# Kernel optimization log

Hardware: AMD Instinct MI355X
Metric: run time of the kernel (lower is better)

## Reference

```python
import jax
import jax.numpy as jnp
import numpy as np


def setup_inputs() -> dict:
    key = jax.random.key(0)
    k1, k2 = jax.random.split(key)
    B, C, H, W = 2, 256, 64, 128  # 1/8-res RAFT features of a 512x1024 image
    fmap1 = jax.random.normal(k1, (B, C, H, W), dtype=jnp.float32)
    fmap2 = jax.random.normal(k2, (B, C, H, W), dtype=jnp.float32)
    return {"fmap1": fmap1, "fmap2": fmap2, "k": 32}


def reference(fmap1, fmap2, k):
    B, C, H, W = fmap1.shape
    N = H * W
    f1 = fmap1.reshape(B, C, N)
    f2 = fmap2.reshape(B, C, N)

    # --- KNN (FAISS inner-product search), indices are non-differentiable ---
    scores = jnp.einsum('bcn,bcm->bnm', jax.lax.stop_gradient(f1),
                        jax.lax.stop_gradient(f2))  # [B, N1, N2]
    _, idx = jax.lax.top_k(scores, k)               # [B, N1, k]
    idx = jnp.transpose(idx, (0, 2, 1))             # [B, k, N1]

    # --- gather top-k target features: gathered[b,c,j,n] = f2[b,c,idx[b,j,n]] ---
    gathered = jax.vmap(lambda f, i: f[:, i])(f2, idx)  # [B, C, k, N1]

    # --- sparse correlation ---
    corr_sp = jnp.einsum('bcn,bckn->bkn', f1, gathered) / jnp.sqrt(jnp.float32(C))

    # --- coordinate grids (y-first), relative displacement ---
    ys, xs = jnp.meshgrid(jnp.arange(H, dtype=jnp.float32),
                          jnp.arange(W, dtype=jnp.float32), indexing='ij')
    coords = jnp.stack([ys.ravel(), xs.ravel()])          # [2, N], y first
    coords0 = jnp.broadcast_to(coords[None, :, None, :], (B, 2, k, N))
    coords1 = jnp.transpose(coords[:, idx], (1, 0, 2, 3))  # [B, 2, k, N]
    coords1 = coords1 - coords0                            # relative offsets

    batch_index = jnp.broadcast_to(
        jnp.arange(B, dtype=jnp.float32).reshape(B, 1, 1, 1), (B, 1, k, N))

    return corr_sp, coords0, coords1, batch_index
```

## Files before the change

kernel.cpp:

```cpp
#include <hip/hip_runtime.h>
#include <hip/hip_bf16.h>

#define B_  2
#define C_  256
#define H_  64
#define W_  128
#define N_  (H_ * W_)
#define K_  32
#define Q_  16
#define CK2 48
#define TN  32
#define TM  32
#define NHT 64

typedef short  short8  __attribute__((ext_vector_type(8)));
typedef short  short4v __attribute__((ext_vector_type(4)));
typedef float  floatx4 __attribute__((ext_vector_type(4)));

__device__ __forceinline__ unsigned umin_(unsigned a, unsigned b) { return a < b ? a : b; }
__device__ __forceinline__ unsigned umax_(unsigned a, unsigned b) { return a > b ? a : b; }
__device__ __forceinline__ ushort f2bf(float v) {
    __hip_bfloat16 h = __float2bfloat16(v);
    ushort u; __builtin_memcpy(&u, &h, 2); return u;
}
__device__ __forceinline__ unsigned med3u(unsigned a, unsigned b, unsigned c) {
    unsigned d;
    asm("v_med3_u32 %0, %1, %2, %3" : "=v"(d) : "v"(a), "v"(b), "v"(c));
    return d;
}

__device__ __forceinline__ unsigned packkey(float v, int m) {
    const float vc = v > 0.0f ? v : 0.0f;
    unsigned b; __builtin_memcpy(&b, &vc, 4);
    return (b & 0xFFFFE000u) | (unsigned)m;
}

__device__ __forceinline__ void qinsert(unsigned (&q)[Q_], unsigned k) {
#pragma unroll
    for (int i = Q_ - 1; i > 0; --i)
        q[i] = med3u(q[i - 1], k, q[i]);
    q[0] = umax_(q[0], k);
}

#define CSWAP(a, b) { const unsigned _mx = umax_(a, b); \
                      const unsigned _mn = umin_(a, b); (a) = _mx; (b) = _mn; }

__global__ void raft_prep_kernel(const float* __restrict__ f1,
                                 const float* __restrict__ f2,
                                 float* __restrict__ f1Tf,
                                 ushort* __restrict__ f2T,
                                 float* __restrict__ f2Tf) {
    __shared__ float tile[32][33];
    const int nt = blockIdx.x;
    const int ct = blockIdx.y;
    const int z  = blockIdx.z;
    const int b  = z >> 1;
    const float* __restrict__ src = (z & 1) ? f2 : f1;
    const int tid = threadIdx.x;

    {
        const int cl = tid >> 3;
        const int nx = tid & 7;
        const float4 v = *(const float4*)(
            src + ((size_t)b * C_ + (ct * 32 + cl)) * N_ + (nt * 32 + nx * 4));
        tile[cl][nx * 4 + 0] = v.x;
        tile[cl][nx * 4 + 1] = v.y;
        tile[cl][nx * 4 + 2] = v.z;
        tile[cl][nx * 4 + 3] = v.w;
    }
    __syncthreads();
    {
        const int nl = tid >> 3;
        const int c4 = (tid & 7) * 4;
        float4 v;
        v.x = tile[c4 + 0][nl];
        v.y = tile[c4 + 1][nl];
        v.z = tile[c4 + 2][nl];
        v.w = tile[c4 + 3][nl];
        const size_t o = ((size_t)b * N_ + (nt * 32 + nl)) * C_ + (ct * 32 + c4);
        if (z & 1) {
            *(float4*)(f2Tf + o) = v;
            short4v h;
            h[0] = (short)f2bf(v.x); h[1] = (short)f2bf(v.y);
            h[2] = (short)f2bf(v.z); h[3] = (short)f2bf(v.w);
            *(short4v*)(f2T + o) = h;
        } else {
            *(float4*)(f1Tf + o) = v;
        }
    }
}

__launch_bounds__(512, 4)
__global__ void raft_stage1_kernel(const float* __restrict__ f1Tf,
                                   const ushort* __restrict__ f2T,
                                   ushort* __restrict__ cand) {
    __shared__ __align__(16) ushort Bt[4][TM * 256];

    const int bid0 = blockIdx.x;
    const int bid  = ((bid0 & 7) << 6) | (bid0 >> 3);
    const int b    = bid >> 8;
    const int nt0  = (bid & 255) * TN;
    const int tid  = threadIdx.x;
    const int w    = tid >> 6;
    const int s    = w & 1;
    const int h    = w >> 1;
    const int lane = tid & 63;
    const int p    = lane & 15;
    const int q4   = lane >> 4;
    const int nrow = nt0 + s * 16 + p;
    const int mbase = h * (N_ / 4);
    const int lt   = tid & 127;

    short8 af[8];
    {
        const float* __restrict__ arow = f1Tf + ((size_t)b * N_ + nrow) * C_;
        #pragma unroll
        for (int ks = 0; ks < 8; ++ks) {
            const float4 x = *(const float4*)(arow + ks * 32 + q4 * 8);
            const float4 y = *(const float4*)(arow + ks * 32 + q4 * 8 + 4);
            short8 t;
            t[0] = (short)f2bf(x.x); t[1] = (short)f2bf(x.y);
            t[2] = (short)f2bf(x.z); t[3] = (short)f2bf(x.w);
            t[4] = (short)f2bf(y.x); t[5] = (short)f2bf(y.y);
            t[6] = (short)f2bf(y.z); t[7] = (short)f2bf(y.w);
            af[ks] = t;
        }
    }

    unsigned q[Q_];
    #pragma unroll
    for (int i = 0; i < Q_; ++i) q[i] = 0u;

    const ushort* __restrict__ Bb = f2T + (size_t)b * N_ * C_ + (size_t)mbase * C_;

    short8 stg[8];
    #pragma unroll
    for (int i = 0; i < 8; ++i) {
        const int idx = lt + 128 * i;
        const int r   = idx >> 5;
        const int c8  = idx & 31;
        stg[i] = *(const short8*)(Bb + (size_t)r * C_ + c8 * 8);
    }

    for (int mt = 0; mt < NHT; ++mt) {
        {
            ushort* __restrict__ dst = Bt[h];
            #pragma unroll
            for (int i = 0; i < 8; ++i) {
                const int idx = lt + 128 * i;
                const int r   = idx >> 5;
                const int c8  = idx & 31;
                *(short8*)(&dst[(r * 32 + (c8 ^ (r & 7))) * 8]) = stg[i];
            }
        }
        __syncthreads();

        if (mt < NHT - 1) {
            const ushort* __restrict__ src = Bb + (size_t)(mt + 1) * TM * C_;
            #pragma unroll
            for (int i = 0; i < 8; ++i) {
                const int idx = lt + 128 * i;
                const int r   = idx >> 5;
                const int c8  = idx & 31;
                stg[i] = *(const short8*)(src + (size_t)r * C_ + c8 * 8);
            }
        }

        const ushort* __restrict__ cur = Bt[h];
        floatx4 acc[2];
        #pragma unroll
        for (int f = 0; f < 2; ++f) acc[f] = (floatx4){0.f, 0.f, 0.f, 0.f};
        #pragma unroll
        for (int ks = 0; ks < 8; ++ks) {
            #pragma unroll
            for (int f = 0; f < 2; ++f) {
                const short8 bm = *(const short8*)(
                    &cur[((f * 16 + p) * 32 + ((ks * 4 + q4) ^ (p & 7))) * 8]);
                acc[f] = __builtin_amdgcn_mfma_f32_16x16x32_bf16(bm, af[ks], acc[f], 0, 0, 0);
            }
        }

        const int m0 = mbase + mt * TM;
        #pragma unroll
        for (int f = 0; f < 2; ++f) {
            const int mb = m0 + f * 16 + q4 * 4;
            unsigned k0 = packkey(acc[f][0], mb + 0);
            unsigned k1 = packkey(acc[f][1], mb + 1);
            unsigned k2 = packkey(acc[f][2], mb + 2);
            unsigned k3 = packkey(acc[f][3], mb + 3);
            CSWAP(k0, k1); CSWAP(k2, k3); CSWAP(k0, k2); CSWAP(k1, k3); CSWAP(k1, k2);
            qinsert(q, k0);
            if (__any(k1 > q[Q_ - 1])) {
                qinsert(q, k1);
                if (__any(k2 > q[Q_ - 1])) {
                    qinsert(q, k2);
                    if (__any(k3 > q[Q_ - 1])) qinsert(q, k3);
                }
            }
        }
        __syncthreads();
    }

    unsigned* __restrict__ mg = (unsigned*)&Bt[0][0];
    const int rowl = s * 16 + p;
    const int qi   = h * 4 + q4;
    #pragma unroll
    for (int t = 0; t < Q_; ++t)
        mg[(qi * Q_ + t) * 33 + rowl] = q[t];
    __syncthreads();

    unsigned* __restrict__ ms = mg + 8448;
    if (tid < 128) {
        const int r = tid >> 2, g = tid & 3;
        const unsigned* __restrict__ Lb = &mg[(g * 4) * Q_ * 33];
        unsigned* __restrict__ O = &ms[(g * 48) * 33 + r];
        int i0 = 0, i1 = 0, i2 = 0, i3 = 0;
        for (int t = 0; t < 48; ++t) {
            const unsigned a0 = (i0 < Q_) ? Lb[(0 * Q_ + i0) * 33 + r] : 0u;
            const unsigned a1 = (i1 < Q_) ? Lb[(1 * Q_ + i1) * 33 + r] : 0u;
            const unsigned a2 = (i2 < Q_) ? Lb[(2 * Q_ + i2) * 33 + r] : 0u;
            const unsigned a3 = (i3 < Q_) ? Lb[(3 * Q_ + i3) * 33 + r] : 0u;
            const unsigned m01 = umax_(a0, a1), m23 = umax_(a2, a3);
            const unsigned mx  = umax_(m01, m23);
            O[t * 33] = mx;
            i0 += (a0 == mx);
            i1 += (a0 != mx) & (a1 == mx);
            i2 += (a0 != mx) & (a1 != mx) & (a2 == mx);
            i3 += (a0 != mx) & (a1 != mx) & (a2 != mx) & (a3 == mx);
        }
    }
    __syncthreads();

    if (tid < 32) {
        int i0 = 0, i1 = 0, i2 = 0, i3 = 0;
        ushort* __restrict__ myc = cand + ((size_t)(b * N_ + nt0 + tid)) * CK2;
        for (int t = 0; t < 48; ++t) {
            const unsigned a0 = ms[(0 * 48 + i0) * 33 + tid];
            const unsigned a1 = ms[(1 * 48 + i1) * 33 + tid];
            const unsigned a2 = ms[(2 * 48 + i2) * 33 + tid];
            const unsigned a3 = ms[(3 * 48 + i3) * 33 + tid];
            const unsigned m01 = umax_(a0, a1), m23 = umax_(a2, a3);
            const unsigned mx  = umax_(m01, m23);
            myc[t] = (ushort)(mx & 0x1FFFu);
            i0 += (a0 == mx);
            i1 += (a0 != mx) & (a1 == mx);
            i2 += (a0 != mx) & (a1 != mx) & (a2 == mx);
            i3 += (a0 != mx) & (a1 != mx) & (a2 != mx) & (a3 == mx);
        }
    }
}

__launch_bounds__(64)
__global__ void raft_rerank_kernel(const float* __restrict__ f1Tf,
                                   const float* __restrict__ f2Tf,
                                   const ushort* __restrict__ cand,
                                   float* __restrict__ out) {
    __shared__ float  aS[C_];
    __shared__ float  cs[CK2];
    __shared__ ushort cmS[CK2];
    const int row = blockIdx.x;
    const int b   = row >> 13;
    const int n   = row & (N_ - 1);
    const int tid = threadIdx.x;

    if (tid < CK2) cmS[tid] = cand[(size_t)row * CK2 + tid];
    *(float4*)(&aS[tid * 4]) = *(const float4*)(f1Tf + ((size_t)b * N_ + n) * C_ + tid * 4);
    __syncthreads();

    if (tid < CK2) {
        const int m = cmS[tid];
        const float* __restrict__ bRow = f2Tf + ((size_t)b * N_ + m) * C_;
        float acc = 0.0f;
        for (int c4 = 0; c4 < C_; c4 += 4) {
            const float4 b4 = *(const float4*)(bRow + c4);
            acc = fmaf(aS[c4 + 0], b4.x, acc);
            acc = fmaf(aS[c4 + 1], b4.y, acc);
            acc = fmaf(aS[c4 + 2], b4.z, acc);
            acc = fmaf(aS[c4 + 3], b4.w, acc);
        }
        cs[tid] = acc;
    }
    __syncthreads();

    const int y0 = n >> 7, x0 = n & 127;
    if (tid < CK2) {
        const float v = cs[tid];
        const int m = cmS[tid];
        int rank = 0;
        for (int j = 0; j < CK2; ++j) {
            const float vj = cs[j];
            rank += (vj > v) || ((vj == v) && (cmS[j] < m));
        }
        if (rank < K_) {
            const size_t posn = (size_t)rank * N_ + n;
            out[(size_t)b * (K_ * N_) + posn] = v * 0.0625f;
            const size_t c1b = (size_t)1572864 + (size_t)b * 2 * K_ * N_;
            out[c1b + posn]                     = (float)((m >> 7) - y0);
            out[c1b + (size_t)(K_ * N_) + posn] = (float)((m & 127) - x0);
        }
    }
    if (tid < K_) {
        const size_t posn = (size_t)tid * N_ + n;
        const size_t c0b = (size_t)524288 + (size_t)b * 2 * K_ * N_;
        out[c0b + posn]                     = (float)y0;
        out[c0b + (size_t)(K_ * N_) + posn] = (float)x0;
        out[(size_t)2621440 + (size_t)b * (K_ * N_) + posn] = (float)b;
    }
}

extern "C" void kernel_launch(void* const* d_in, const int* in_sizes, int n_in,
                              void* d_out, int out_size, void* d_ws, size_t ws_size,
                              hipStream_t stream) {
    const float* f1 = (const float*)d_in[0];
    const float* f2 = (const float*)d_in[1];

    float*  f1Tf = (float*)d_ws;
    float*  f2Tf = f1Tf + (size_t)B_ * N_ * C_;
    ushort* f2T  = (ushort*)(f2Tf + (size_t)B_ * N_ * C_);
    ushort* cand = f2T + (size_t)B_ * N_ * C_;

    raft_prep_kernel<<<dim3(N_ / 32, C_ / 32, B_ * 2), dim3(256), 0, stream>>>(
        f1, f2, f1Tf, f2T, f2Tf);

    raft_stage1_kernel<<<dim3(B_ * (N_ / TN)), dim3(512), 0, stream>>>(f1Tf, f2T, cand);

    raft_rerank_kernel<<<dim3(B_ * N_), dim3(64), 0, stream>>>(f1Tf, f2Tf, cand,
                                                               (float*)d_out);
}
```

Before: 378.8 us.

## Shrink rerank candidates, batch rows per rerank block, relax stage1 barriers

The candidate count passed from the bf16 MFMA stage to the fp32 rerank drops from 48 to 36, which shrinks the merge loops and the rerank work. The rerank kernel now handles 16 rows per 576-thread block instead of one row per 64-thread block, with a swizzled block index. In stage 1 the first barrier moves after the next-tile global prefetch, and both barriers become a raw LDS-wait plus s_barrier. Fewer candidates raise the chance that a true top-32 neighbour is lost to bf16 rounding in the first pass.

```diff
diff --git a/kernel.cpp b/kernel.cpp
--- a/kernel.cpp
+++ b/kernel.cpp
@@ -8,10 +8,11 @@
 #define N_  (H_ * W_)
 #define K_  32
 #define Q_  16
-#define CK2 48
+#define CK2 36
 #define TN  32
 #define TM  32
 #define NHT 64
+#define RR  16
 
 typedef short  short8  __attribute__((ext_vector_type(8)));
 typedef short  short4v __attribute__((ext_vector_type(4)));
@@ -44,6 +45,13 @@
 
 #define CSWAP(a, b) { const unsigned _mx = umax_(a, b); \
                       const unsigned _mn = umin_(a, b); (a) = _mx; (b) = _mn; }
+
+__device__ __forceinline__ void bar_lgkm() {
+    asm volatile("s_waitcnt lgkmcnt(0)" ::: "memory");
+    __builtin_amdgcn_sched_barrier(0);
+    __builtin_amdgcn_s_barrier();
+    __builtin_amdgcn_sched_barrier(0);
+}
 
 __global__ void raft_prep_kernel(const float* __restrict__ f1,
                                  const float* __restrict__ f2,
@@ -153,7 +161,6 @@
                 *(short8*)(&dst[(r * 32 + (c8 ^ (r & 7))) * 8]) = stg[i];
             }
         }
-        __syncthreads();
 
         if (mt < NHT - 1) {
             const ushort* __restrict__ src = Bb + (size_t)(mt + 1) * TM * C_;
@@ -165,6 +172,7 @@
                 stg[i] = *(const short8*)(src + (size_t)r * C_ + c8 * 8);
             }
         }
+        bar_lgkm();
 
         const ushort* __restrict__ cur = Bt[h];
         floatx4 acc[2];
@@ -198,7 +206,7 @@
                 }
             }
         }
-        __syncthreads();
+        bar_lgkm();
     }
 
     unsigned* __restrict__ mg = (unsigned*)&Bt[0][0];
@@ -213,9 +221,9 @@
     if (tid < 128) {
         const int r = tid >> 2, g = tid & 3;
         const unsigned* __restrict__ Lb = &mg[(g * 4) * Q_ * 33];
-        unsigned* __restrict__ O = &ms[(g * 48) * 33 + r];
+        unsigned* __restrict__ O = &ms[(g * CK2) * 33 + r];
         int i0 = 0, i1 = 0, i2 = 0, i3 = 0;
-        for (int t = 0; t < 48; ++t) {
+        for (int t = 0; t < CK2; ++t) {
             const unsigned a0 = (i0 < Q_) ? Lb[(0 * Q_ + i0) * 33 + r] : 0u;
             const unsigned a1 = (i1 < Q_) ? Lb[(1 * Q_ + i1) * 33 + r] : 0u;
             const unsigned a2 = (i2 < Q_) ? Lb[(2 * Q_ + i2) * 33 + r] : 0u;
@@ -234,11 +242,11 @@
     if (tid < 32) {
         int i0 = 0, i1 = 0, i2 = 0, i3 = 0;
         ushort* __restrict__ myc = cand + ((size_t)(b * N_ + nt0 + tid)) * CK2;
-        for (int t = 0; t < 48; ++t) {
-            const unsigned a0 = ms[(0 * 48 + i0) * 33 + tid];
-            const unsigned a1 = ms[(1 * 48 + i1) * 33 + tid];
-            const unsigned a2 = ms[(2 * 48 + i2) * 33 + tid];
-            const unsigned a3 = ms[(3 * 48 + i3) * 33 + tid];
+        for (int t = 0; t < CK2; ++t) {
+            const unsigned a0 = ms[(0 * CK2 + i0) * 33 + tid];
+            const unsigned a1 = ms[(1 * CK2 + i1) * 33 + tid];
+            const unsigned a2 = ms[(2 * CK2 + i2) * 33 + tid];
+            const unsigned a3 = ms[(3 * CK2 + i3) * 33 + tid];
             const unsigned m01 = umax_(a0, a1), m23 = umax_(a2, a3);
             const unsigned mx  = umax_(m01, m23);
             myc[t] = (ushort)(mx & 0x1FFFu);
@@ -250,61 +258,74 @@
     }
 }
 
-__launch_bounds__(64)
+__launch_bounds__(576)
 __global__ void raft_rerank_kernel(const float* __restrict__ f1Tf,
                                    const float* __restrict__ f2Tf,
                                    const ushort* __restrict__ cand,
                                    float* __restrict__ out) {
-    __shared__ float  aS[C_];
-    __shared__ float  cs[CK2];
-    __shared__ ushort cmS[CK2];
-    const int row = blockIdx.x;
-    const int b   = row >> 13;
-    const int n   = row & (N_ - 1);
-    const int tid = threadIdx.x;
-
-    if (tid < CK2) cmS[tid] = cand[(size_t)row * CK2 + tid];
-    *(float4*)(&aS[tid * 4]) = *(const float4*)(f1Tf + ((size_t)b * N_ + n) * C_ + tid * 4);
-    __syncthreads();
-
-    if (tid < CK2) {
-        const int m = cmS[tid];
-        const float* __restrict__ bRow = f2Tf + ((size_t)b * N_ + m) * C_;
+    __shared__ float  aS[RR][C_];
+    __shared__ float  cs[RR][CK2];
+    __shared__ ushort cmS[RR][CK2];
+    const int bid0 = blockIdx.x;
+    const int bid  = ((bid0 & 7) << 7) | (bid0 >> 3);
+    const int row0 = bid * RR;
+    const int tid  = threadIdx.x;
+    const int r    = tid / CK2;
+    const int c    = tid - r * CK2;
+
+    for (int sidx = tid; sidx < RR * (C_ / 4); sidx += RR * CK2) {
+        const int rr = sidx >> 6, s4 = sidx & 63;
+        const int rg = row0 + rr;
+        const int bb = rg >> 13, nn = rg & (N_ - 1);
+        *(float4*)(&aS[rr][s4 * 4]) =
+            *(const float4*)(f1Tf + ((size_t)bb * N_ + nn) * C_ + s4 * 4);
+    }
+    cmS[r][c] = cand[(size_t)(row0 + r) * CK2 + c];
+    __syncthreads();
+
+    {
+        const int rg = row0 + r;
+        const int bb = rg >> 13;
+        const int m  = cmS[r][c];
+        const float* __restrict__ bRow = f2Tf + ((size_t)bb * N_ + m) * C_;
         float acc = 0.0f;
         for (int c4 = 0; c4 < C_; c4 += 4) {
             const float4 b4 = *(const float4*)(bRow + c4);
-            acc = fmaf(aS[c4 + 0], b4.x, acc);
-            acc = fmaf(aS[c4 + 1], b4.y, acc);
-            acc = fmaf(aS[c4 + 2], b4.z, acc);
-            acc = fmaf(aS[c4 + 3], b4.w, acc);
-        }
-        cs[tid] = acc;
-    }
-    __syncthreads();
-
+            acc = fmaf(aS[r][c4 + 0], b4.x, acc);
+            acc = fmaf(aS[r][c4 + 1], b4.y, acc);
+            acc = fmaf(aS[r][c4 + 2], b4.z, acc);
+            acc = fmaf(aS[r][c4 + 3], b4.w, acc);
+        }
+        cs[r][c] = acc;
+    }
+    __syncthreads();
+
+    const int rg = row0 + r;
+    const int bb = rg >> 13;
+    const int n  = rg & (N_ - 1);
     const int y0 = n >> 7, x0 = n & 127;
-    if (tid < CK2) {
-        const float v = cs[tid];
-        const int m = cmS[tid];
+    {
+        const float v = cs[r][c];
+        const int m = cmS[r][c];
         int rank = 0;
         for (int j = 0; j < CK2; ++j) {
-            const float vj = cs[j];
-            rank += (vj > v) || ((vj == v) && (cmS[j] < m));
+            const float vj = cs[r][j];
+            rank += (vj > v) || ((vj == v) && (cmS[r][j] < m));
         }
         if (rank < K_) {
             const size_t posn = (size_t)rank * N_ + n;
-            out[(size_t)b * (K_ * N_) + posn] = v * 0.0625f;
-            const size_t c1b = (size_t)1572864 + (size_t)b * 2 * K_ * N_;
+            out[(size_t)bb * (K_ * N_) + posn] = v * 0.0625f;
+            const size_t c1b = (size_t)1572864 + (size_t)bb * 2 * K_ * N_;
             out[c1b + posn]                     = (float)((m >> 7) - y0);
             out[c1b + (size_t)(K_ * N_) + posn] = (float)((m & 127) - x0);
         }
     }
-    if (tid < K_) {
-        const size_t posn = (size_t)tid * N_ + n;
-        const size_t c0b = (size_t)524288 + (size_t)b * 2 * K_ * N_;
+    if (c < K_) {
+        const size_t posn = (size_t)c * N_ + n;
+        const size_t c0b = (size_t)524288 + (size_t)bb * 2 * K_ * N_;
         out[c0b + posn]                     = (float)y0;
         out[c0b + (size_t)(K_ * N_) + posn] = (float)x0;
-        out[(size_t)2621440 + (size_t)b * (K_ * N_) + posn] = (float)b;
+        out[(size_t)2621440 + (size_t)bb * (K_ * N_) + posn] = (float)bb;
     }
 }
 
@@ -324,6 +345,6 @@
 
     raft_stage1_kernel<<<dim3(B_ * (N_ / TN)), dim3(512), 0, stream>>>(f1Tf, f2T, cand);
 
-    raft_rerank_kernel<<<dim3(B_ * N_), dim3(64), 0, stream>>>(f1Tf, f2Tf, cand,
-                                                               (float*)d_out);
-}
+    raft_rerank_kernel<<<dim3(B_ * N_ / RR), dim3(RR * CK2), 0, stream>>>(
+        f1Tf, f2Tf, cand, (float*)d_out);
+}
```

Measured after the change: 347.9 us. 8.2% less time.
